# Performance work log

Hardware: AMD Instinct MI355X
Metric: run time of the kernel (lower is better)

Reference implementation:

```python
import jax, jax.numpy as jnp
import numpy as np
from jax import lax

# Grid / module constants (from init_kwargs)
D = 128        # spatial extent per axis (shape=[128,128,128])
CIN = 16       # in_channels
COUT = 32      # out_channels
K = 2          # kernel_size
S = 2          # stride
B = 2          # batch_size
N = 200000     # number of active voxels


def setup_inputs() -> dict:
    key = jax.random.key(0)
    k1, k2, k3, k4 = jax.random.split(key, 4)
    features = jax.random.normal(k1, (N, CIN), dtype=jnp.float32)
    coors = jax.random.randint(k2, (N, 4), 0, D)                  # [b, z, y, x]
    coors = coors.at[:, 0].set(coors[:, 0] % B)                    # batch ids in [0, B)
    # Learned params: SCN Convolution / Deconvolution weights (bias=False).
    W1 = jax.random.normal(k3, (COUT, CIN, K, K, K), dtype=jnp.float32) * 0.1
    W2 = jax.random.normal(k4, (CIN, COUT, K, K, K), dtype=jnp.float32) * 0.1
    return {"features": features, "W1": W1, "W2": W2, "coors": coors, "batch_size": B}


def reference(features, W1, W2, coors, batch_size):
    # scn.InputLayer: scatter point features onto the sparse voxel grid
    # (duplicate coords are summed). Inactive sites are exactly zero, so a
    # dense strided conv computes the same values as the rulebook
    # gather-GEMM-scatter at every active output site.
    b, z, y, x = coors[:, 0], coors[:, 1], coors[:, 2], coors[:, 3]
    dense = jnp.zeros((batch_size, CIN, D, D, D), dtype=features.dtype)
    dense = dense.at[b, :, z, y, x].add(features)                  # [B, CIN, D, D, D]

    dn = ("NCDHW", "OIDHW", "NCDHW")
    # scn.Convolution(ndim, CIN, COUT, K, S): valid strided conv -> [B, COUT, D//S, ...]
    h = lax.conv_general_dilated(dense, W1, window_strides=(S, S, S),
                                 padding="VALID", dimension_numbers=dn)
    # scn.Deconvolution(ndim, COUT, CIN, K, S): transposed conv back to [B, CIN, D, D, D]
    dec = lax.conv_general_dilated(h, W2, window_strides=(1, 1, 1),
                                   padding=[(K - 1, K - 1)] * 3,
                                   lhs_dilation=(S, S, S), dimension_numbers=dn)
    # Coupled deconv in SCN restores exactly the input active set; SparseToDense
    # then writes zeros everywhere else -> mask to the original active sites.
    mask = jnp.zeros((batch_size, 1, D, D, D), dtype=features.dtype)
    mask = mask.at[b, :, z, y, x].set(1.0)
    return dec * mask
```

## Files before the change

### kernel.cpp

```cpp
#include <hip/hip_runtime.h>
#include <stdint.h>

#define H_BYTES   ((size_t)67108864)
#define MASK_OFF  ((size_t)67108864)
#define CNT_OFF   ((size_t)67633152)
#define BASE_OFF  ((size_t)67633408)
#define WL_OFF    ((size_t)68157696)
#define VALS_OFF  ((size_t)69206272)
#define PITCH     262144
#define NWORDS    131072

typedef float f32x4 __attribute__((ext_vector_type(4)));

__global__ __launch_bounds__(256) void scn_scatter_conv1(
    const float* __restrict__ feat, const float* __restrict__ W1,
    const int* __restrict__ coors, float* __restrict__ h,
    uint32_t* __restrict__ maskw, int npts)
{
    __shared__ float Ws[8 * 16 * 32];
    for (int i = threadIdx.x; i < 4096; i += 256) {
        int ic = i >> 7, rem = i & 127, cin = rem >> 3, p = rem & 7;
        Ws[(p << 9) | (cin << 5) | ic] = W1[i];
    }
    __syncthreads();

    int total = npts * 32;
    for (int idx = blockIdx.x * 256 + threadIdx.x; idx < total;
         idx += gridDim.x * 256) {
        int pid = idx >> 5, ic = idx & 31;
        int b = coors[pid * 4 + 0];
        int z = coors[pid * 4 + 1];
        int y = coors[pid * 4 + 2];
        int x = coors[pid * 4 + 3];
        int p = ((z & 1) << 2) | ((y & 1) << 1) | (x & 1);

        const f32x4* f4 = reinterpret_cast<const f32x4*>(feat + pid * 16);
        f32x4 a0 = f4[0], a1 = f4[1], a2 = f4[2], a3 = f4[3];

        const float* w = Ws + (p << 9) + ic;
        float s = 0.f;
        s += a0[0] * w[0 << 5];   s += a0[1] * w[1 << 5];
        s += a0[2] * w[2 << 5];   s += a0[3] * w[3 << 5];
        s += a1[0] * w[4 << 5];   s += a1[1] * w[5 << 5];
        s += a1[2] * w[6 << 5];   s += a1[3] * w[7 << 5];
        s += a2[0] * w[8 << 5];   s += a2[1] * w[9 << 5];
        s += a2[2] * w[10 << 5];  s += a2[3] * w[11 << 5];
        s += a3[0] * w[12 << 5];  s += a3[1] * w[13 << 5];
        s += a3[2] * w[14 << 5];  s += a3[3] * w[15 << 5];

        int cell = (b << 18) | ((z >> 1) << 12) | ((y >> 1) << 6) | (x >> 1);
        atomicAdd(&h[((size_t)cell << 5) | ic], s);

        if (ic == 0) {
            int voxel = (z << 14) | (y << 7) | x;
            atomicOr(&maskw[(b << 16) | (voxel >> 5)], 1u << (voxel & 31));
        }
    }
}

__global__ __launch_bounds__(256) void scn_base_worklist(
    const uint32_t* __restrict__ maskw, uint32_t* __restrict__ basew,
    uint32_t* __restrict__ wl, uint32_t* __restrict__ cnt)
{
    int i = blockIdx.x * 256 + threadIdx.x;
    if (i >= NWORDS) return;
    uint32_t w = maskw[i];
    if (!w) return;
    int n = __popc(w);
    uint32_t b = atomicAdd(cnt, (uint32_t)n);
    basew[i] = b;
    uint32_t vbase = (uint32_t)i << 5;
    while (w) {
        int bit = __ffs(w) - 1;
        wl[b++] = vbase | (uint32_t)bit;
        w &= w - 1;
    }
}

__global__ __launch_bounds__(256) void scn_compute_vals(
    const float* __restrict__ h, const float* __restrict__ W2,
    const uint32_t* __restrict__ wl, const uint32_t* __restrict__ cnt,
    float* __restrict__ vals)
{
    __shared__ float Ws[8 * 529];
    for (int i = threadIdx.x; i < 4096; i += 256) {
        int oc = i >> 8, rem = i & 255, ic = rem >> 3, p = rem & 7;
        Ws[p * 529 + (ic << 4) + oc] = W2[i];
    }
    __syncthreads();

    uint32_t n = *cnt;
    uint32_t i = blockIdx.x * 256 + threadIdx.x;
    if (i >= n) return;

    uint32_t v = wl[i];
    int b = v >> 21, z = (v >> 14) & 127, y = (v >> 7) & 127, x = v & 127;
    int p = (((z & 1) ^ 1) << 2) | (((y & 1) ^ 1) << 1) | ((x & 1) ^ 1);
    int cell = (b << 18) | ((z >> 1) << 12) | ((y >> 1) << 6) | (x >> 1);

    const f32x4* hc = reinterpret_cast<const f32x4*>(h + ((size_t)cell << 5));
    f32x4 hv[8];
    #pragma unroll
    for (int q = 0; q < 8; ++q) hv[q] = hc[q];

    const float* wp = Ws + p * 529;
    for (int oc = 0; oc < 16; ++oc) {
        float s = 0.f;
        #pragma unroll
        for (int q = 0; q < 8; ++q) {
            s += hv[q][0] * wp[((4 * q + 0) << 4) + oc];
            s += hv[q][1] * wp[((4 * q + 1) << 4) + oc];
            s += hv[q][2] * wp[((4 * q + 2) << 4) + oc];
            s += hv[q][3] * wp[((4 * q + 3) << 4) + oc];
        }
        vals[(size_t)oc * PITCH + i] = s;
    }
}

__global__ __launch_bounds__(256) void scn_fill_merge(
    const uint32_t* __restrict__ maskw, const uint32_t* __restrict__ basew,
    const float* __restrict__ vals, float* __restrict__ out)
{
    const int total4 = 16777216;
    int stride = gridDim.x * 256;
    for (int o = blockIdx.x * 256 + threadIdx.x; o < total4; o += stride) {
        int voxel4 = o & 524287;
        int chan   = o >> 19;
        int b = chan >> 4;
        int word = (b << 16) | (voxel4 >> 3);
        uint32_t mword = maskw[word];
        uint32_t nib = (mword >> ((voxel4 & 7) << 2)) & 0xFu;

        f32x4 r = {0.f, 0.f, 0.f, 0.f};
        if (nib) {
            const float* voc = vals + ((size_t)(chan & 15) << 18);
            uint32_t base = basew[word];
            int bit0 = (voxel4 & 7) << 2;
            #pragma unroll
            for (int j = 0; j < 4; ++j) {
                if ((nib >> j) & 1u) {
                    uint32_t rank = __popc(mword & ((1u << (bit0 + j)) - 1u));
                    r[j] = voc[base + rank];
                }
            }
        }
        __builtin_nontemporal_store(r, reinterpret_cast<f32x4*>(out) + o);
    }
}

extern "C" void kernel_launch(void* const* d_in, const int* in_sizes, int n_in,
                              void* d_out, int out_size, void* d_ws, size_t ws_size,
                              hipStream_t stream) {
    const float* feat  = (const float*)d_in[0];
    const float* W1    = (const float*)d_in[1];
    const float* W2    = (const float*)d_in[2];
    const int*   coors = (const int*)d_in[3];
    float*       out   = (float*)d_out;

    char* ws = (char*)d_ws;
    float*    h     = (float*)ws;
    uint32_t* maskw = (uint32_t*)(ws + MASK_OFF);
    uint32_t* cnt   = (uint32_t*)(ws + CNT_OFF);
    uint32_t* basew = (uint32_t*)(ws + BASE_OFF);
    uint32_t* wl    = (uint32_t*)(ws + WL_OFF);
    float*    vals  = (float*)(ws + VALS_OFF);
    int npts = in_sizes[0] / 16;

    hipMemsetAsync(d_ws, 0, CNT_OFF + 256, stream);

    int t1 = npts * 32;
    int blocks1 = (t1 + 255) / 256;
    if (blocks1 > 4096) blocks1 = 4096;
    scn_scatter_conv1<<<blocks1, 256, 0, stream>>>(feat, W1, coors, h, maskw, npts);

    scn_base_worklist<<<NWORDS / 256, 256, 0, stream>>>(maskw, basew, wl, cnt);

    scn_compute_vals<<<1024, 256, 0, stream>>>(h, W2, wl, cnt, vals);

    scn_fill_merge<<<2048, 256, 0, stream>>>(maskw, basew, vals, out);
}
```

Before: 392.8 us.

## Use ordered prefix-scan worklist and shared-memory staged fill

Replaces the atomic-counter worklist build with a three-kernel prefix scan, so active voxels are numbered in mask order and each mask word's base index grows monotonically. The final fill kernel can then give each block one contiguous 8K-voxel chunk and stage that chunk's mask, base and value entries in shared memory. Output is written with regular stores instead of nontemporal ones. The goal is to turn scattered global gathers of vals into coalesced loads; the cost is two extra kernel launches and one block-wide barrier stage per chunk.

```diff
diff --git a/kernel.cpp b/kernel.cpp
--- a/kernel.cpp
+++ b/kernel.cpp
@@ -1,12 +1,12 @@
 #include <hip/hip_runtime.h>
 #include <stdint.h>
 
-#define H_BYTES   ((size_t)67108864)
 #define MASK_OFF  ((size_t)67108864)
 #define CNT_OFF   ((size_t)67633152)
-#define BASE_OFF  ((size_t)67633408)
-#define WL_OFF    ((size_t)68157696)
-#define VALS_OFF  ((size_t)69206272)
+#define BSUM_OFF  ((size_t)67633408)
+#define BASE_OFF  ((size_t)67637504)
+#define WL_OFF    ((size_t)68161792)
+#define VALS_OFF  ((size_t)69210368)
 #define PITCH     262144
 #define NWORDS    131072
 
@@ -58,21 +58,61 @@
     }
 }
 
-__global__ __launch_bounds__(256) void scn_base_worklist(
-    const uint32_t* __restrict__ maskw, uint32_t* __restrict__ basew,
-    uint32_t* __restrict__ wl, uint32_t* __restrict__ cnt)
-{
-    int i = blockIdx.x * 256 + threadIdx.x;
-    if (i >= NWORDS) return;
+__global__ __launch_bounds__(256) void scn_scan1(
+    const uint32_t* __restrict__ maskw, uint32_t* __restrict__ bsum)
+{
+    __shared__ uint32_t red[256];
+    int t = threadIdx.x;
+    red[t] = __popc(maskw[blockIdx.x * 256 + t]);
+    __syncthreads();
+    for (int s = 128; s > 0; s >>= 1) {
+        if (t < s) red[t] += red[t + s];
+        __syncthreads();
+    }
+    if (t == 0) bsum[blockIdx.x] = red[0];
+}
+
+__global__ __launch_bounds__(512) void scn_scan2(
+    uint32_t* __restrict__ bsum, uint32_t* __restrict__ cnt)
+{
+    __shared__ uint32_t v[512];
+    int t = threadIdx.x;
+    v[t] = bsum[t];
+    __syncthreads();
+    for (int off = 1; off < 512; off <<= 1) {
+        uint32_t x = v[t];
+        uint32_t y = (t >= off) ? v[t - off] : 0;
+        __syncthreads();
+        v[t] = x + y;
+        __syncthreads();
+    }
+    bsum[t] = t ? v[t - 1] : 0;
+    if (t == 511) *cnt = v[511];
+}
+
+__global__ __launch_bounds__(256) void scn_scan3(
+    const uint32_t* __restrict__ maskw, const uint32_t* __restrict__ bsum,
+    uint32_t* __restrict__ basew, uint32_t* __restrict__ wl)
+{
+    __shared__ uint32_t v[256];
+    int t = threadIdx.x;
+    int i = blockIdx.x * 256 + t;
     uint32_t w = maskw[i];
-    if (!w) return;
-    int n = __popc(w);
-    uint32_t b = atomicAdd(cnt, (uint32_t)n);
-    basew[i] = b;
-    uint32_t vbase = (uint32_t)i << 5;
+    v[t] = __popc(w);
+    __syncthreads();
+    for (int off = 1; off < 256; off <<= 1) {
+        uint32_t x = v[t];
+        uint32_t y = (t >= off) ? v[t - off] : 0;
+        __syncthreads();
+        v[t] = x + y;
+        __syncthreads();
+    }
+    uint32_t base = bsum[blockIdx.x] + (t ? v[t - 1] : 0);
+    basew[i] = base;
+    uint32_t vb = (uint32_t)i << 5;
     while (w) {
         int bit = __ffs(w) - 1;
-        wl[b++] = vbase | (uint32_t)bit;
+        wl[base++] = vb | (uint32_t)bit;
         w &= w - 1;
     }
 }
@@ -121,30 +161,46 @@
     const uint32_t* __restrict__ maskw, const uint32_t* __restrict__ basew,
     const float* __restrict__ vals, float* __restrict__ out)
 {
-    const int total4 = 16777216;
-    int stride = gridDim.x * 256;
-    for (int o = blockIdx.x * 256 + threadIdx.x; o < total4; o += stride) {
-        int voxel4 = o & 524287;
-        int chan   = o >> 19;
-        int b = chan >> 4;
-        int word = (b << 16) | (voxel4 >> 3);
-        uint32_t mword = maskw[word];
-        uint32_t nib = (mword >> ((voxel4 & 7) << 2)) & 0xFu;
-
+    __shared__ uint32_t s_mask[256];
+    __shared__ uint32_t s_base[256];
+    __shared__ float    s_vals[8192];
+
+    int tid   = threadIdx.x;
+    int chunk = blockIdx.x;
+    int chan  = chunk >> 8;
+    int c     = chunk & 255;
+    int b     = chan >> 4;
+    int oc    = chan & 15;
+
+    int w0 = (b << 16) | (c << 8);
+    s_mask[tid] = maskw[w0 + tid];
+    s_base[tid] = basew[w0 + tid];
+    __syncthreads();
+
+    uint32_t vbase = s_base[0];
+    uint32_t vend  = s_base[255] + __popc(s_mask[255]);
+    int n = (int)(vend - vbase);
+    const float* voc = vals + ((size_t)oc << 18);
+    for (int i = tid; i < n; i += 256) s_vals[i] = voc[vbase + i];
+    __syncthreads();
+
+    f32x4* out4 = reinterpret_cast<f32x4*>(out) + ((size_t)chan << 19)
+                + (size_t)c * 2048;
+    #pragma unroll
+    for (int it = 0; it < 8; ++it) {
+        int lv4 = it * 256 + tid;
+        uint32_t mword = s_mask[lv4 >> 3];
+        int bit0 = (lv4 & 7) << 2;
+        uint32_t nib = (mword >> bit0) & 0xFu;
         f32x4 r = {0.f, 0.f, 0.f, 0.f};
         if (nib) {
-            const float* voc = vals + ((size_t)(chan & 15) << 18);
-            uint32_t base = basew[word];
-            int bit0 = (voxel4 & 7) << 2;
-            #pragma unroll
-            for (int j = 0; j < 4; ++j) {
-                if ((nib >> j) & 1u) {
-                    uint32_t rank = __popc(mword & ((1u << (bit0 + j)) - 1u));
-                    r[j] = voc[base + rank];
-                }
-            }
+            uint32_t base = s_base[lv4 >> 3] - vbase;
+            if (nib & 1u) r[0] = s_vals[base + __popc(mword & ((1u << (bit0 + 0)) - 1u))];
+            if (nib & 2u) r[1] = s_vals[base + __popc(mword & ((1u << (bit0 + 1)) - 1u))];
+            if (nib & 4u) r[2] = s_vals[base + __popc(mword & ((1u << (bit0 + 2)) - 1u))];
+            if (nib & 8u) r[3] = s_vals[base + __popc(mword & ((1u << (bit0 + 3)) - 1u))];
         }
-        __builtin_nontemporal_store(r, reinterpret_cast<f32x4*>(out) + o);
+        out4[lv4] = r;
     }
 }
 
@@ -161,21 +217,24 @@
     float*    h     = (float*)ws;
     uint32_t* maskw = (uint32_t*)(ws + MASK_OFF);
     uint32_t* cnt   = (uint32_t*)(ws + CNT_OFF);
+    uint32_t* bsum  = (uint32_t*)(ws + BSUM_OFF);
     uint32_t* basew = (uint32_t*)(ws + BASE_OFF);
     uint32_t* wl    = (uint32_t*)(ws + WL_OFF);
     float*    vals  = (float*)(ws + VALS_OFF);
     int npts = in_sizes[0] / 16;
 
-    hipMemsetAsync(d_ws, 0, CNT_OFF + 256, stream);
+    hipMemsetAsync(d_ws, 0, CNT_OFF, stream);
 
     int t1 = npts * 32;
     int blocks1 = (t1 + 255) / 256;
     if (blocks1 > 4096) blocks1 = 4096;
     scn_scatter_conv1<<<blocks1, 256, 0, stream>>>(feat, W1, coors, h, maskw, npts);
 
-    scn_base_worklist<<<NWORDS / 256, 256, 0, stream>>>(maskw, basew, wl, cnt);
+    scn_scan1<<<NWORDS / 256, 256, 0, stream>>>(maskw, bsum);
+    scn_scan2<<<1, 512, 0, stream>>>(bsum, cnt);
+    scn_scan3<<<NWORDS / 256, 256, 0, stream>>>(maskw, bsum, basew, wl);
 
     scn_compute_vals<<<1024, 256, 0, stream>>>(h, W2, wl, cnt, vals);
 
-    scn_fill_merge<<<2048, 256, 0, stream>>>(maskw, basew, vals, out);
-}
+    scn_fill_merge<<<8192, 256, 0, stream>>>(maskw, basew, vals, out);
+}
```

After: 364.2 us. 7.3% less time.
